# Kernel optimization log

Measured on AMD Instinct MI355X. Metric: run time of the kernel, lower is better.

Reference implementation:

```python
import jax, jax.numpy as jnp
import numpy as np

N_NODES = 50000
N_EDGES = 800000
NODE_DIM = 128
EDGE_DIM = 10
IN_DIM = 2 * NODE_DIM + EDGE_DIM
BN_EPS = 1e-5


def setup_inputs() -> dict:
    key = jax.random.key(0)
    ks = jax.random.split(key, 8)
    h = jax.random.normal(ks[0], (N_NODES, NODE_DIM), dtype=jnp.float32)
    edge_index = jax.random.randint(ks[1], (2, N_EDGES), 0, N_NODES, dtype=jnp.int64)
    edge_feat = jax.random.normal(ks[2], (N_EDGES, EDGE_DIM), dtype=jnp.float32)
    scale = 1.0 / np.sqrt(IN_DIM)
    gate_w = jax.random.normal(ks[3], (IN_DIM, NODE_DIM), dtype=jnp.float32) * scale
    gate_b = jax.random.normal(ks[4], (NODE_DIM,), dtype=jnp.float32) * scale
    cand_w = jax.random.normal(ks[5], (IN_DIM, NODE_DIM), dtype=jnp.float32) * scale
    cand_b = jax.random.normal(ks[6], (NODE_DIM,), dtype=jnp.float32) * scale
    bn_gamma = jnp.ones((NODE_DIM,), dtype=jnp.float32)
    bn_beta = jnp.zeros((NODE_DIM,), dtype=jnp.float32)
    return {"h": h, "edge_index": edge_index, "edge_feat": edge_feat,
            "gate_w": gate_w, "gate_b": gate_b, "cand_w": cand_w, "cand_b": cand_b,
            "bn_gamma": bn_gamma, "bn_beta": bn_beta}


def reference(h, edge_index, edge_feat, gate_w, gate_b, cand_w, cand_b, bn_gamma, bn_beta):
    src = edge_index[0]
    dst = edge_index[1]
    # gather endpoint features and concat with edge features: [E, 2*D + De]
    z = jnp.concatenate([h[src], h[dst], edge_feat], axis=1)
    g = jax.nn.sigmoid(z @ gate_w + gate_b)   # [E, D]
    c = jax.nn.softplus(z @ cand_w + cand_b)  # [E, D]
    m = g * c
    # scatter-add messages to source nodes (matches index_add_(0, src, m))
    agg = jax.ops.segment_sum(m, src, num_segments=h.shape[0])
    # BatchNorm1d in training mode: batch mean / biased variance over nodes
    mean = jnp.mean(agg, axis=0)
    var = jnp.var(agg, axis=0)
    agg_bn = (agg - mean) * jax.lax.rsqrt(var + BN_EPS) * bn_gamma + bn_beta
    return jax.nn.softplus(h + agg_bn)
```

## Files before the change

kernel.cpp:

```cpp
#include <hip/hip_runtime.h>
#include <math.h>

#define N_NODES 50000
#define N_EDGES 800000
#define D 128
#define DE 10
#define TE 64
#define N_TILES (N_EDGES / TE)
#define SST 132
#define ASTR 136
#define OST 520
#define WP2_ELEMS (4 * 32 * 64 * 8)
#define WEF_ELEMS (16 * 64 * 8)
#define SCAN_BLOCKS 196
#define CSTRIDE 16
#define SCAT_BLOCKS 1563
#define GEMM_BLOCKS 782

typedef __bf16 bf16x8 __attribute__((ext_vector_type(8)));
typedef __bf16 bf16x4 __attribute__((ext_vector_type(4)));
typedef __bf16 bf16x2 __attribute__((ext_vector_type(2)));
typedef float  f32x4  __attribute__((ext_vector_type(4)));
typedef unsigned int u32x4 __attribute__((ext_vector_type(4)));

__device__ __forceinline__ float fast_sigmoid(float x) {
    float t = __builtin_amdgcn_exp2f(-1.44269504089f * x);
    return __builtin_amdgcn_rcpf(1.0f + t);
}
__device__ __forceinline__ float fast_softplus(float x) {
    float t = __builtin_amdgcn_exp2f(-1.44269504089f * fabsf(x));
    return fmaxf(x, 0.0f) + 0.69314718056f * __builtin_amdgcn_logf(1.0f + t);
}
__device__ __forceinline__ float bflo(unsigned int u) {
    return __builtin_bit_cast(float, u << 16);
}
__device__ __forceinline__ float bfhi(unsigned int u) {
    return __builtin_bit_cast(float, u & 0xFFFF0000u);
}

__global__ __launch_bounds__(256) void prep(
    const float* __restrict__ gw, const float* __restrict__ cw,
    const int* __restrict__ ei,
    __bf16* __restrict__ wp2, __bf16* __restrict__ wef,
    int* __restrict__ counts, unsigned char* __restrict__ rank)
{
    int bx = blockIdx.x, t = threadIdx.x;
    if (bx < 256) {
        int idx = bx * 256 + t;
        int j    = idx & 7;
        int lane = (idx >> 3) & 63;
        int nb   = (idx >> 9) & 31;
        int kb   = idx >> 14;
        int k    = kb * 32 + ((lane >> 4) << 3) + j;
        int jp   = nb * 16 + (lane & 15);
        float v;
        if      (jp < 128) v = gw[k * D + jp];
        else if (jp < 256) v = cw[k * D + (jp - 128)];
        else if (jp < 384) v = gw[(128 + k) * D + (jp - 256)];
        else               v = cw[(128 + k) * D + (jp - 384)];
        wp2[idx] = (__bf16)v;
    } else if (bx < 288) {
        int idx = (bx - 256) * 256 + t;
        int j    = idx & 7;
        int lane = (idx >> 3) & 63;
        int nb   = idx >> 9;
        int k    = ((lane >> 4) << 3) + j;
        int col  = (nb >> 1) * 16 + (lane & 15);
        const float* w = (nb & 1) ? cw : gw;
        wef[idx] = (__bf16)((k < 10) ? w[(256 + k) * D + col] : 0.0f);
    } else {
        int e = (bx - 288) * 256 + t;
        int r = atomicAdd(&counts[ei[e] * CSTRIDE], 1);
        rank[e] = (unsigned char)r;
    }
}

__global__ __launch_bounds__(256) void scan_partials(
    const int* __restrict__ counts, int* __restrict__ bsum)
{
    __shared__ int ss[256];
    int t = threadIdx.x;
    int i = blockIdx.x * 256 + t;
    int c = (i < N_NODES) ? counts[i * CSTRIDE] : 0;
    ss[t] = c;
    __syncthreads();
    #pragma unroll
    for (int off = 1; off < 256; off <<= 1) {
        int v = (t >= off) ? ss[t - off] : 0;
        __syncthreads();
        ss[t] += v;
        __syncthreads();
    }
    if (t == 255) bsum[blockIdx.x] = ss[255];
}

__global__ __launch_bounds__(256) void scan_final(
    const int* __restrict__ counts, const int* __restrict__ bsum,
    int* __restrict__ anchors, unsigned short* __restrict__ excl16)
{
    __shared__ int sb[256];
    __shared__ int ss[256];
    int t = threadIdx.x;
    sb[t] = (t < SCAN_BLOCKS) ? bsum[t] : 0;
    int i = blockIdx.x * 256 + t;
    int c = (i < N_NODES) ? counts[i * CSTRIDE] : 0;
    ss[t] = c;
    __syncthreads();
    #pragma unroll
    for (int off = 1; off < 256; off <<= 1) {
        int v  = (t >= off) ? ss[t - off] : 0;
        int vb = (t >= off) ? sb[t - off] : 0;
        __syncthreads();
        ss[t] += v;
        sb[t] += vb;
        __syncthreads();
    }
    if (t == 0) anchors[blockIdx.x] = blockIdx.x ? sb[blockIdx.x - 1] : 0;
    if (i < N_NODES) excl16[i] = (unsigned short)(ss[t] - c);
}

__global__ __launch_bounds__(512, 4) void scatter_gemm(
    const int* __restrict__ ei, const unsigned char* __restrict__ rank,
    const int* __restrict__ anchors, const unsigned short* __restrict__ excl16,
    unsigned int* __restrict__ sdx, unsigned short* __restrict__ eidlo,
    unsigned char* __restrict__ eidhi,
    const float* __restrict__ h, const __bf16* __restrict__ wp2,
    unsigned int* __restrict__ paI, unsigned int* __restrict__ pbI)
{
    if (blockIdx.x < SCAT_BLOCKS) {
        int e = blockIdx.x * 512 + threadIdx.x;
        if (e < N_EDGES) {
            int node = ei[e];
            int pos = anchors[node >> 8] + (int)excl16[node] + (int)rank[e];
            sdx[pos]   = (unsigned int)node | ((unsigned int)ei[N_EDGES + e] << 16);
            eidlo[pos] = (unsigned short)e;
            eidhi[pos] = (unsigned char)(e >> 16);
        }
        return;
    }

    __shared__ __align__(16) __bf16 sm[64 * OST];
    __bf16* za = sm;
    const int t  = threadIdx.x;
    const int r0 = (blockIdx.x - SCAT_BLOCKS) * 64;

    #pragma unroll
    for (int it = 0; it < 4; ++it) {
        int ch  = it * 512 + t;
        int row = ch >> 5, cs = ch & 31;
        int node = r0 + row;
        float4 v = (node < N_NODES) ? *(const float4*)&h[(size_t)node * D + cs * 4]
                                    : make_float4(0.f, 0.f, 0.f, 0.f);
        bf16x4 o = { (__bf16)v.x, (__bf16)v.y, (__bf16)v.z, (__bf16)v.w };
        *(bf16x4*)&za[row * ASTR + cs * 4] = o;
    }
    __syncthreads();

    const int w = t >> 6, l = t & 63, quad = l >> 4, col16 = l & 15;
    f32x4 acc[4][4];
    #pragma unroll
    for (int mt = 0; mt < 4; ++mt)
        #pragma unroll
        for (int nt = 0; nt < 4; ++nt)
            acc[mt][nt] = (f32x4)0.0f;

    const __bf16* zp = &za[col16 * ASTR + quad * 8];
    const __bf16* bp = &wp2[(size_t)((w * 4) * 64 + l) * 8];

    #pragma unroll
    for (int kb = 0; kb < 4; ++kb) {
        bf16x8 afr[4];
        #pragma unroll
        for (int mt = 0; mt < 4; ++mt)
            afr[mt] = *(const bf16x8*)&zp[mt * 16 * ASTR + kb * 32];
        bf16x8 bfr[4];
        #pragma unroll
        for (int nt = 0; nt < 4; ++nt)
            bfr[nt] = *(const bf16x8*)&bp[(size_t)(kb * 32 + nt) * 512];
        #pragma unroll
        for (int mt = 0; mt < 4; ++mt)
            #pragma unroll
            for (int nt = 0; nt < 4; ++nt)
                acc[mt][nt] = __builtin_amdgcn_mfma_f32_16x16x32_bf16(
                    afr[mt], bfr[nt], acc[mt][nt], 0, 0, 0);
    }
    __syncthreads();

    #pragma unroll
    for (int mt = 0; mt < 4; ++mt)
        #pragma unroll
        for (int nt = 0; nt < 4; ++nt)
            #pragma unroll
            for (int r = 0; r < 4; ++r) {
                int row  = mt * 16 + quad * 4 + r;
                int colj = (w * 4 + nt) * 16 + col16;
                sm[row * OST + colj] = (__bf16)acc[mt][nt][r];
            }
    __syncthreads();

    #pragma unroll
    for (int it = 0; it < 8; ++it) {
        int ch   = it * 512 + t;
        int row  = ch >> 6;
        int sub  = ch & 63;
        int hp   = sub >> 5;
        int c0   = (sub & 31) * 4;
        int node = r0 + row;
        if (node < N_NODES) {
            const __bf16* sr = &sm[row * OST + hp * 256];
            bf16x4 gl = *(const bf16x4*)&sr[c0];
            bf16x4 cl = *(const bf16x4*)&sr[128 + c0];
            unsigned int wds[4];
            #pragma unroll
            for (int i = 0; i < 4; ++i) {
                bf16x2 pr = { gl[i], cl[i] };
                wds[i] = __builtin_bit_cast(unsigned int, pr);
            }
            unsigned int* dp = hp ? pbI : paI;
            *(uint4*)&dp[(size_t)node * 128 + c0] = *(const uint4*)&wds[0];
        }
    }
}

__global__ __launch_bounds__(512, 6) void edge_fuse(
    const unsigned int* __restrict__ paI, const unsigned int* __restrict__ pbI,
    const unsigned int* __restrict__ sdx, const unsigned short* __restrict__ eidlo,
    const unsigned char* __restrict__ eidhi,
    const float* __restrict__ ef, const __bf16* __restrict__ wef,
    const float* __restrict__ gb, const float* __restrict__ cb,
    float* __restrict__ agg)
{
    __shared__ __align__(16) unsigned int sbuf[TE * SST];
    __shared__ __align__(16) __bf16 zE[TE * 32];
    __shared__ int s_src[TE], s_dst[TE];

    const int t  = threadIdx.x;
    const int e0 = blockIdx.x * TE;
    const int w = t >> 6, l = t & 63, quad = l >> 4, col16 = l & 15;

    const __bf16* wpp = &wef[(size_t)((w * 2) * 64 + l) * 8];
    bf16x8 bfr0 = *(const bf16x8*)&wpp[0];
    bf16x8 bfr1 = *(const bf16x8*)&wpp[512];
    const int c = w * 16 + col16;
    const float gbv = gb[c], cbv = cb[c];

    if (t < TE) {
        unsigned int sd = sdx[e0 + t];
        int eid = (int)eidlo[e0 + t] | ((int)eidhi[e0 + t] << 16);
        s_src[t] = (int)(sd & 0xFFFFu);
        s_dst[t] = (int)(sd >> 16);
        const float* efr = &ef[(size_t)eid * DE];
        __bf16* row = &zE[t * 32];
        #pragma unroll
        for (int j = 0; j < 5; ++j) {
            float2 a = *(const float2*)&efr[j * 2];
            bf16x2 pr = { (__bf16)a.x, (__bf16)a.y };
            *(bf16x2*)&row[j * 2] = pr;
        }
        *(bf16x2*)&row[10] = (bf16x2)(__bf16)0.0f;
        *(bf16x4*)&row[12] = (bf16x4)(__bf16)0.0f;
        *(bf16x8*)&row[16] = (bf16x8)(__bf16)0.0f;
        *(bf16x8*)&row[24] = (bf16x8)(__bf16)0.0f;
    }
    __syncthreads();

    #pragma unroll
    for (int it = 0; it < 2; ++it) {
        int id  = it * 512 + t;
        int e   = id >> 4, grp = id & 15;
        int src = s_src[e], dst = s_dst[e];
        int c0  = grp * 8;
        u32x4 a0 = *(const u32x4*)&paI[(size_t)src * 128 + c0];
        u32x4 a1 = *(const u32x4*)&paI[(size_t)src * 128 + c0 + 4];
        u32x4 b0 = *(const u32x4*)&pbI[(size_t)dst * 128 + c0];
        u32x4 b1 = *(const u32x4*)&pbI[(size_t)dst * 128 + c0 + 4];
        unsigned int o[8];
        #pragma unroll
        for (int j = 0; j < 4; ++j) {
            bf16x2 p0 = { (__bf16)(bflo(a0[j]) + bflo(b0[j])),
                          (__bf16)(bfhi(a0[j]) + bfhi(b0[j])) };
            bf16x2 p1 = { (__bf16)(bflo(a1[j]) + bflo(b1[j])),
                          (__bf16)(bfhi(a1[j]) + bfhi(b1[j])) };
            o[j]     = __builtin_bit_cast(unsigned int, p0);
            o[j + 4] = __builtin_bit_cast(unsigned int, p1);
        }
        *(uint4*)&sbuf[e * SST + c0]     = *(const uint4*)&o[0];
        *(uint4*)&sbuf[e * SST + c0 + 4] = *(const uint4*)&o[4];
    }
    __syncthreads();

    const f32x4 bg4 = { gbv, gbv, gbv, gbv };
    const f32x4 bc4 = { cbv, cbv, cbv, cbv };
    f32x4 accg[4], accc[4];
    #pragma unroll
    for (int mt = 0; mt < 4; ++mt) {
        const bf16x8 a = *(const bf16x8*)&zE[(mt * 16 + col16) * 32 + quad * 8];
        accg[mt] = __builtin_amdgcn_mfma_f32_16x16x32_bf16(a, bfr0, bg4, 0, 0, 0);
        accc[mt] = __builtin_amdgcn_mfma_f32_16x16x32_bf16(a, bfr1, bc4, 0, 0, 0);
    }

    #pragma unroll
    for (int mt = 0; mt < 4; ++mt) {
        #pragma unroll
        for (int r = 0; r < 4; ++r) {
            int e = mt * 16 + quad * 4 + r;
            unsigned int u = sbuf[e * SST + c];
            float g = bflo(u) + accg[mt][r];
            float x = bfhi(u) + accc[mt][r];
            ((float*)sbuf)[e * SST + c] = fast_sigmoid(g) * fast_softplus(x);
        }
    }
    __syncthreads();

    const int seg = t >> 7;
    const int cc  = t & 127;
    const int rlo = seg * 16, rhi = rlo + 16;
    int   cur = s_src[rlo];
    float s   = 0.0f;
    const float* ms = (const float*)sbuf;
    for (int e = rlo; e < rhi; ++e) {
        int node = s_src[e];
        float v  = ms[e * SST + cc];
        if (node != cur) {
            atomicAdd(&agg[(size_t)cur * D + cc], s);
            s = 0.0f; cur = node;
        }
        s += v;
    }
    atomicAdd(&agg[(size_t)cur * D + cc], s);
}

__global__ __launch_bounds__(256) void col_stats(
    const float* __restrict__ agg, float* __restrict__ stats)
{
    const int t    = threadIdx.x;
    const int col  = t & 127;
    const int half = t >> 7;
    float s = 0.0f, s2 = 0.0f;
    for (int r = blockIdx.x * 2 + half; r < N_NODES; r += gridDim.x * 2) {
        float v = agg[(size_t)r * D + col];
        s += v; s2 += v * v;
    }
    atomicAdd(&stats[col], s);
    atomicAdd(&stats[128 + col], s2);
}

__global__ __launch_bounds__(256) void out_softplus(
    const float* __restrict__ h, const float* __restrict__ agg,
    const float* __restrict__ stats, const float* __restrict__ gamma,
    const float* __restrict__ beta, float* __restrict__ out)
{
    __shared__ float sc[128], bi[128];
    int t = threadIdx.x;
    if (t < 128) {
        const float inv_n = 1.0f / (float)N_NODES;
        float mean = stats[t] * inv_n;
        float var  = stats[128 + t] * inv_n - mean * mean;
        var = fmaxf(var, 0.0f);
        float rstd = rsqrtf(var + 1e-5f);
        float s = rstd * gamma[t];
        sc[t] = s;
        bi[t] = beta[t] - mean * s;
    }
    __syncthreads();
    int idx4 = blockIdx.x * 256 + t;
    int base = idx4 * 4;
    if (base < N_NODES * D) {
        float4 hv = *(const float4*)&h[base];
        float4 av = *(const float4*)&agg[base];
        int c = base & 127;
        float4 o;
        o.x = fast_softplus(hv.x + av.x * sc[c + 0] + bi[c + 0]);
        o.y = fast_softplus(hv.y + av.y * sc[c + 1] + bi[c + 1]);
        o.z = fast_softplus(hv.z + av.z * sc[c + 2] + bi[c + 2]);
        o.w = fast_softplus(hv.w + av.w * sc[c + 3] + bi[c + 3]);
        *(float4*)&out[base] = o;
    }
}

extern "C" void kernel_launch(void* const* d_in, const int* in_sizes, int n_in,
                              void* d_out, int out_size, void* d_ws, size_t ws_size,
                              hipStream_t stream) {
    const float* h     = (const float*)d_in[0];
    const int*   ei    = (const int*)  d_in[1];
    const float* ef    = (const float*)d_in[2];
    const float* gw    = (const float*)d_in[3];
    const float* gb    = (const float*)d_in[4];
    const float* cw    = (const float*)d_in[5];
    const float* cb    = (const float*)d_in[6];
    const float* gamma = (const float*)d_in[7];
    const float* beta  = (const float*)d_in[8];
    float* out = (float*)d_out;

    float*          agg     = (float*)d_ws;
    float*          stats   = agg + (size_t)N_NODES * D;
    int*            counts  = (int*)(stats + 256);
    unsigned int*   pbI     = (unsigned int*)counts;
    char*           afterU  = (char*)counts + (size_t)N_NODES * 128 * sizeof(unsigned int);
    __bf16*         wp2     = (__bf16*)afterU;
    __bf16*         wef     = wp2 + WP2_ELEMS;
    int*            bsum    = (int*)(wef + WEF_ELEMS);
    int*            anchors = bsum + 256;
    unsigned short* excl16  = (unsigned short*)(anchors + 256);
    unsigned char*  rank    = (unsigned char*)(excl16 + N_NODES);
    unsigned int*   sdx     = (unsigned int*)(rank + N_EDGES);
    unsigned short* eidlo   = (unsigned short*)(sdx + N_EDGES);
    unsigned char*  eidhi   = (unsigned char*)(eidlo + N_EDGES);
    unsigned int*   paI     = (unsigned int*)d_out;

    const size_t zero_bytes = ((size_t)N_NODES * D + 256) * sizeof(float)
                            + (size_t)N_NODES * CSTRIDE * sizeof(int);
    hipMemsetAsync(d_ws, 0, zero_bytes, stream);
    prep<<<3413, 256, 0, stream>>>(gw, cw, ei, wp2, wef, counts, rank);
    scan_partials<<<SCAN_BLOCKS, 256, 0, stream>>>(counts, bsum);
    scan_final<<<SCAN_BLOCKS, 256, 0, stream>>>(counts, bsum, anchors, excl16);
    scatter_gemm<<<SCAT_BLOCKS + GEMM_BLOCKS, 512, 0, stream>>>(
        ei, rank, anchors, excl16, sdx, eidlo, eidhi, h, wp2, paI, pbI);
    edge_fuse<<<N_TILES, 512, 0, stream>>>(
        paI, pbI, sdx, eidlo, eidhi, ef, wef, gb, cb, agg);
    col_stats<<<784, 256, 0, stream>>>(agg, stats);
    out_softplus<<<N_NODES * D / 4 / 256, 256, 0, stream>>>(
        h, agg, stats, gamma, beta, out);
}
```

Before: 341.0 us.

## Merge scan and finish kernels with cooperative grid sync; zero agg in prep

Folds the two scan kernels into one cooperative kernel separated by a grid-wide sync, and merges column statistics and the output softplus into a single cooperative kernel. Zeroing of the aggregation buffer moves from a memset into extra blocks of the prep kernel, and stats atomics are first reduced within each block. This cuts kernel launches and launch gaps, at the cost of grid-sync overhead and a grid-stride output loop that runs on fewer blocks.

```diff
diff --git a/kernel.cpp b/kernel.cpp
--- a/kernel.cpp
+++ b/kernel.cpp
@@ -1,5 +1,8 @@
 #include <hip/hip_runtime.h>
+#include <hip/hip_cooperative_groups.h>
 #include <math.h>
+
+namespace cg = cooperative_groups;
 
 #define N_NODES 50000
 #define N_EDGES 800000
@@ -16,6 +19,7 @@
 #define CSTRIDE 16
 #define SCAT_BLOCKS 1563
 #define GEMM_BLOCKS 782
+#define FIN_BLOCKS 784
 
 typedef __bf16 bf16x8 __attribute__((ext_vector_type(8)));
 typedef __bf16 bf16x4 __attribute__((ext_vector_type(4)));
@@ -42,7 +46,8 @@
     const float* __restrict__ gw, const float* __restrict__ cw,
     const int* __restrict__ ei,
     __bf16* __restrict__ wp2, __bf16* __restrict__ wef,
-    int* __restrict__ counts, unsigned char* __restrict__ rank)
+    int* __restrict__ counts, unsigned char* __restrict__ rank,
+    float4* __restrict__ aggz)
 {
     int bx = blockIdx.x, t = threadIdx.x;
     if (bx < 256) {
@@ -68,20 +73,26 @@
         int col  = (nb >> 1) * 16 + (lane & 15);
         const float* w = (nb & 1) ? cw : gw;
         wef[idx] = (__bf16)((k < 10) ? w[(256 + k) * D + col] : 0.0f);
-    } else {
+    } else if (bx < 3413) {
         int e = (bx - 288) * 256 + t;
         int r = atomicAdd(&counts[ei[e] * CSTRIDE], 1);
         rank[e] = (unsigned char)r;
-    }
-}
-
-__global__ __launch_bounds__(256) void scan_partials(
-    const int* __restrict__ counts, int* __restrict__ bsum)
+    } else {
+        int i = (bx - 3413) * 256 + t;
+        aggz[i] = make_float4(0.f, 0.f, 0.f, 0.f);
+    }
+}
+
+__global__ __launch_bounds__(256) void scan_both(
+    const int* __restrict__ counts, int* __restrict__ bsum,
+    int* __restrict__ anchors, unsigned short* __restrict__ excl16)
 {
+    cg::grid_group grid = cg::this_grid();
     __shared__ int ss[256];
-    int t = threadIdx.x;
-    int i = blockIdx.x * 256 + t;
-    int c = (i < N_NODES) ? counts[i * CSTRIDE] : 0;
+    __shared__ int sb[256];
+    const int t = threadIdx.x, b = blockIdx.x;
+    const int i = b * 256 + t;
+    const int c = (i < N_NODES) ? counts[i * CSTRIDE] : 0;
     ss[t] = c;
     __syncthreads();
     #pragma unroll
@@ -91,31 +102,19 @@
         ss[t] += v;
         __syncthreads();
     }
-    if (t == 255) bsum[blockIdx.x] = ss[255];
-}
-
-__global__ __launch_bounds__(256) void scan_final(
-    const int* __restrict__ counts, const int* __restrict__ bsum,
-    int* __restrict__ anchors, unsigned short* __restrict__ excl16)
-{
-    __shared__ int sb[256];
-    __shared__ int ss[256];
-    int t = threadIdx.x;
+    if (t == 255) bsum[b] = ss[255];
+    grid.sync();
+
     sb[t] = (t < SCAN_BLOCKS) ? bsum[t] : 0;
-    int i = blockIdx.x * 256 + t;
-    int c = (i < N_NODES) ? counts[i * CSTRIDE] : 0;
-    ss[t] = c;
     __syncthreads();
     #pragma unroll
     for (int off = 1; off < 256; off <<= 1) {
-        int v  = (t >= off) ? ss[t - off] : 0;
-        int vb = (t >= off) ? sb[t - off] : 0;
+        int v = (t >= off) ? sb[t - off] : 0;
         __syncthreads();
-        ss[t] += v;
-        sb[t] += vb;
+        sb[t] += v;
         __syncthreads();
     }
-    if (t == 0) anchors[blockIdx.x] = blockIdx.x ? sb[blockIdx.x - 1] : 0;
+    if (t == 0) anchors[b] = b ? sb[b - 1] : 0;
     if (i < N_NODES) excl16[i] = (unsigned short)(ss[t] - c);
 }
 
@@ -330,28 +329,33 @@
     atomicAdd(&agg[(size_t)cur * D + cc], s);
 }
 
-__global__ __launch_bounds__(256) void col_stats(
-    const float* __restrict__ agg, float* __restrict__ stats)
+__global__ __launch_bounds__(256) void finish(
+    const float* __restrict__ h, const float* __restrict__ agg,
+    float* __restrict__ stats, const float* __restrict__ gamma,
+    const float* __restrict__ beta, float* __restrict__ out)
 {
-    const int t    = threadIdx.x;
+    cg::grid_group grid = cg::this_grid();
+    const int t = threadIdx.x;
     const int col  = t & 127;
     const int half = t >> 7;
-    float s = 0.0f, s2 = 0.0f;
-    for (int r = blockIdx.x * 2 + half; r < N_NODES; r += gridDim.x * 2) {
-        float v = agg[(size_t)r * D + col];
-        s += v; s2 += v * v;
-    }
-    atomicAdd(&stats[col], s);
-    atomicAdd(&stats[128 + col], s2);
-}
-
-__global__ __launch_bounds__(256) void out_softplus(
-    const float* __restrict__ h, const float* __restrict__ agg,
-    const float* __restrict__ stats, const float* __restrict__ gamma,
-    const float* __restrict__ beta, float* __restrict__ out)
-{
+
+    __shared__ float rs[128], rq[128];
+    {
+        float s = 0.0f, s2 = 0.0f;
+        for (int r = blockIdx.x * 2 + half; r < N_NODES; r += gridDim.x * 2) {
+            float v = agg[(size_t)r * D + col];
+            s += v; s2 += v * v;
+        }
+        if (half == 1) { rs[col] = s; rq[col] = s2; }
+        __syncthreads();
+        if (half == 0) {
+            atomicAdd(&stats[col],       s  + rs[col]);
+            atomicAdd(&stats[128 + col], s2 + rq[col]);
+        }
+    }
+    grid.sync();
+
     __shared__ float sc[128], bi[128];
-    int t = threadIdx.x;
     if (t < 128) {
         const float inv_n = 1.0f / (float)N_NODES;
         float mean = stats[t] * inv_n;
@@ -363,17 +367,17 @@
         bi[t] = beta[t] - mean * s;
     }
     __syncthreads();
-    int idx4 = blockIdx.x * 256 + t;
-    int base = idx4 * 4;
-    if (base < N_NODES * D) {
+    const int total4 = N_NODES * D / 4;
+    for (int idx4 = blockIdx.x * 256 + t; idx4 < total4; idx4 += gridDim.x * 256) {
+        int base = idx4 * 4;
         float4 hv = *(const float4*)&h[base];
         float4 av = *(const float4*)&agg[base];
-        int c = base & 127;
+        int cc = base & 127;
         float4 o;
-        o.x = fast_softplus(hv.x + av.x * sc[c + 0] + bi[c + 0]);
-        o.y = fast_softplus(hv.y + av.y * sc[c + 1] + bi[c + 1]);
-        o.z = fast_softplus(hv.z + av.z * sc[c + 2] + bi[c + 2]);
-        o.w = fast_softplus(hv.w + av.w * sc[c + 3] + bi[c + 3]);
+        o.x = fast_softplus(hv.x + av.x * sc[cc + 0] + bi[cc + 0]);
+        o.y = fast_softplus(hv.y + av.y * sc[cc + 1] + bi[cc + 1]);
+        o.z = fast_softplus(hv.z + av.z * sc[cc + 2] + bi[cc + 2]);
+        o.w = fast_softplus(hv.w + av.w * sc[cc + 3] + bi[cc + 3]);
         *(float4*)&out[base] = o;
     }
 }
@@ -407,18 +411,26 @@
     unsigned short* eidlo   = (unsigned short*)(sdx + N_EDGES);
     unsigned char*  eidhi   = (unsigned char*)(eidlo + N_EDGES);
     unsigned int*   paI     = (unsigned int*)d_out;
-
-    const size_t zero_bytes = ((size_t)N_NODES * D + 256) * sizeof(float)
-                            + (size_t)N_NODES * CSTRIDE * sizeof(int);
-    hipMemsetAsync(d_ws, 0, zero_bytes, stream);
-    prep<<<3413, 256, 0, stream>>>(gw, cw, ei, wp2, wef, counts, rank);
-    scan_partials<<<SCAN_BLOCKS, 256, 0, stream>>>(counts, bsum);
-    scan_final<<<SCAN_BLOCKS, 256, 0, stream>>>(counts, bsum, anchors, excl16);
+    float4*         aggz    = (float4*)agg;
+
+    hipMemsetAsync(stats, 0,
+                   256 * sizeof(float) + (size_t)N_NODES * CSTRIDE * sizeof(int),
+                   stream);
+    prep<<<9663, 256, 0, stream>>>(gw, cw, ei, wp2, wef, counts, rank, aggz);
+    {
+        void* args[] = { (void*)&counts, (void*)&bsum, (void*)&anchors,
+                         (void*)&excl16 };
+        hipLaunchCooperativeKernel((const void*)scan_both,
+                                   dim3(SCAN_BLOCKS), dim3(256), args, 0, stream);
+    }
     scatter_gemm<<<SCAT_BLOCKS + GEMM_BLOCKS, 512, 0, stream>>>(
         ei, rank, anchors, excl16, sdx, eidlo, eidhi, h, wp2, paI, pbI);
     edge_fuse<<<N_TILES, 512, 0, stream>>>(
         paI, pbI, sdx, eidlo, eidhi, ef, wef, gb, cb, agg);
-    col_stats<<<784, 256, 0, stream>>>(agg, stats);
-    out_softplus<<<N_NODES * D / 4 / 256, 256, 0, stream>>>(
-        h, agg, stats, gamma, beta, out);
-}
+    {
+        void* args[] = { (void*)&h, (void*)&agg, (void*)&stats,
+                         (void*)&gamma, (void*)&beta, (void*)&out };
+        hipLaunchCooperativeKernel((const void*)finish,
+                                   dim3(FIN_BLOCKS), dim3(256), args, 0, stream);
+    }
+}
```

After: 403.4 us. +18.3%, slower.
